# Kernel tuning notes

Measured on AMD Instinct MI355X. Metric: run time of the kernel, lower is better.

## Reference

```python
import jax, jax.numpy as jnp
import numpy as np

BN_EPS = 1e-5
ITER_N = 5

def _bn(x, gamma, beta, mean, var, axis):
    shape = [1] * x.ndim
    shape[axis] = -1
    r = lambda v: v.reshape(shape)
    return (x - r(mean)) * (r(gamma) / jnp.sqrt(r(var) + BN_EPS)) + r(beta)

def _covpool(x):
    # x: (B, d, M); MPNCOV CovpoolLayer: y = x @ I_hat @ x^T, I_hat = (1/M)I - (1/M^2)11^T
    M = x.shape[-1]
    I_hat = (-1.0 / (M * M)) * jnp.ones((M, M), x.dtype) + (1.0 / M) * jnp.eye(M, dtype=x.dtype)
    return jnp.einsum('bdm,mn,ben->bde', x, I_hat, x)

def _sqrtm_ns(A, iterN=ITER_N):
    # MPNCOV SqrtmLayer: trace-normalized Newton-Schulz iteration
    d = A.shape[-1]
    I3 = 3.0 * jnp.eye(d, dtype=A.dtype)
    normA = jnp.trace(A, axis1=1, axis2=2) / 3.0          # (B,)
    A_n = A / normA[:, None, None]
    ZY = 0.5 * (I3 - A_n)
    Y = A_n @ ZY
    Z = ZY
    for _ in range(iterN - 2):
        ZY = 0.5 * (I3 - Z @ Y)
        Y = Y @ ZY
        Z = ZY @ Z
    YZY = 0.5 * (Y @ (I3 - Z @ Y))
    return YZY * jnp.sqrt(normA)[:, None, None]

def setup_inputs() -> dict:
    key = jax.random.key(0)
    ks = jax.random.split(key, 12)
    B, C, H, W = 64, 1024, 16, 16
    D, R = 128, H * W  # att_dim, sp_reso
    return {
        'x': jax.random.normal(ks[0], (B, C, H, W), jnp.float32),
        'w_dr': jax.random.normal(ks[1], (D, C), jnp.float32) * 0.02,
        'b_dr': jax.random.normal(ks[2], (D,), jnp.float32) * 0.02,
        'bn1_gamma': jnp.ones((D,), jnp.float32),
        'bn1_beta': jnp.zeros((D,), jnp.float32),
        'bn1_mean': jax.random.normal(ks[3], (D,), jnp.float32) * 0.1,
        'bn1_var': jax.random.uniform(ks[4], (D,), jnp.float32, 0.5, 1.5),
        'bn2_gamma': jnp.ones((R,), jnp.float32),
        'bn2_beta': jnp.zeros((R,), jnp.float32),
        'bn2_mean': jax.random.normal(ks[5], (R,), jnp.float32) * 0.1,
        'bn2_var': jax.random.uniform(ks[6], (R,), jnp.float32, 0.5, 1.5),
        'rc_w': jax.random.normal(ks[7], (R,), jnp.float32) * 0.1 + 1.0,
        'rc_b': jax.random.normal(ks[8], (R,), jnp.float32) * 0.02,
        'fc_w': jax.random.normal(ks[9], (R, R * R), jnp.float32) * 0.004,
        'fc_b': jax.random.normal(ks[10], (R,), jnp.float32) * 0.02,
    }

def reference(x, w_dr, b_dr, bn1_gamma, bn1_beta, bn1_mean, bn1_var,
              bn2_gamma, bn2_beta, bn2_mean, bn2_var, rc_w, rc_b, fc_w, fc_b):
    B, C, H, W = x.shape
    # 1x1 dimension-reduction conv + BN + ReLU
    y = jnp.einsum('bchw,dc->bdhw', x, w_dr) + b_dr[None, :, None, None]
    y = jax.nn.relu(_bn(y, bn1_gamma, bn1_beta, bn1_mean, bn1_var, axis=1))
    # (B, D, HW) -> (B, HW, D): HW spatial positions as 'channels', D as samples
    y = y.reshape(B, -1, H * W).transpose(0, 2, 1)
    cov = _covpool(y)                  # (B, HW, HW)
    s = _sqrtm_ns(cov, ITER_N)         # (B, HW, HW)
    # row BN over first HW axis (channels of the (B, HW, HW, 1) view)
    s = _bn(s, bn2_gamma, bn2_beta, bn2_mean, bn2_var, axis=1)
    # grouped (depthwise) 1x1 row conv: per-row scale + bias
    s = s * rc_w[None, :, None] + rc_b[None, :, None]
    att = jax.nn.sigmoid(s.reshape(B, -1) @ fc_w.T + fc_b)   # (B, HW)
    att = att.reshape(B, 1, H, W)
    return x * att
```

## Files before the change

### kernel.cpp

```cpp
#include <hip/hip_runtime.h>

typedef unsigned short u16;
typedef unsigned int   u32;
typedef __attribute__((ext_vector_type(8))) short bf8;
typedef __attribute__((ext_vector_type(4))) float f4;
typedef __attribute__((ext_vector_type(16))) float f16f;

#define MFMA(a,b,c)   __builtin_amdgcn_mfma_f32_16x16x32_bf16(a,b,c,0,0,0)
#define MFMA32(a,b,c) __builtin_amdgcn_mfma_f32_32x32x16_bf16(a,b,c,0,0,0)

__device__ __forceinline__ u16 f2bf(float f){
  u32 u = __float_as_uint(f);
  u += 0x7fffu + ((u >> 16) & 1u);
  return (u16)(u >> 16);
}
__device__ __forceinline__ float bf2f(u16 h){ return __uint_as_float(((u32)h) << 16); }
__device__ __forceinline__ u32 pk2(float a, float b){ return (u32)f2bf(a) | ((u32)f2bf(b) << 16); }

__device__ __forceinline__ bf8 ldsFrag(const char* m, int row0, int k0, int pitch){
  int l = threadIdx.x & 63;
  int r = row0 + (l & 15);
  int kb = ((k0 + ((l >> 4) << 3)) << 1) ^ ((r & 7) << 4);
  return *(const bf8*)(m + r * pitch + kb);
}
__device__ __forceinline__ void ldsPut(char* m, int row, int col, int pitch, u16 v){
  int kb = (col << 1) ^ ((row & 7) << 4);
  *(u16*)(m + row * pitch + kb) = v;
}

__device__ __forceinline__ bf8 fragNS(const char* m, int r0, int ks, int l){
  int r = r0 + (l & 31);
  int kb = ((ks << 5) + ((l >> 5) << 4)) ^ ((r & 15) << 4);
  return *(const bf8*)(m + r * 256 + kb);
}
__device__ __forceinline__ bf8 fragWT(const char* m, int r0, int ks, int l){
  int r = r0 + (l & 31);
  int kb = ((ks << 5) + ((l >> 5) << 4)) ^ ((r & 15) << 4);
  return *(const bf8*)(m + r * 512 + kb);
}
__device__ __forceinline__ char* nsAddr(char* m, int row, int col4){
  return m + row * 256 + ((col4 << 1) ^ ((row & 15) << 4));
}

__device__ __forceinline__ void mmPass(const char* A, const char* B, f16f (&acc)[2][2],
                                       int R0, int C0, int l){
  #pragma unroll
  for (int ks = 0; ks < 8; ++ks){
    bf8 a0 = fragNS(A, R0,      ks, l);
    bf8 a1 = fragNS(A, R0 + 32, ks, l);
    bf8 b0 = fragNS(B, C0,      ks, l);
    bf8 b1 = fragNS(B, C0 + 32, ks, l);
    acc[0][0] = MFMA32(a0, b0, acc[0][0]); acc[0][1] = MFMA32(a0, b1, acc[0][1]);
    acc[1][0] = MFMA32(a1, b0, acc[1][0]); acc[1][1] = MFMA32(a1, b1, acc[1][1]);
  }
}

__device__ __forceinline__ void writeTile(char* D, const f16f (&acc)[2][2], int R0, int C0, int l,
                                          float scale, float dval, const uint2* adv){
  #pragma unroll
  for (int ri = 0; ri < 2; ++ri)
  #pragma unroll
  for (int ci = 0; ci < 2; ++ci)
  #pragma unroll
  for (int g = 0; g < 4; ++g){
    int srow = C0 + ci * 32 + (l & 31);
    int scol = R0 + ri * 32 + g * 8 + ((l >> 5) << 2);
    float v[4];
    #pragma unroll
    for (int q = 0; q < 4; ++q){
      float x = scale * acc[ri][ci][g * 4 + q];
      x += ((scol + q) == srow) ? dval : 0.f;
      v[q] = x;
    }
    if (adv){
      uint2 ad = adv[(ri * 2 + ci) * 4 + g];
      v[0] += 1.5f * bf2f((u16)ad.x);
      v[1] += 1.5f * bf2f((u16)(ad.x >> 16));
      v[2] += 1.5f * bf2f((u16)ad.y);
      v[3] += 1.5f * bf2f((u16)(ad.y >> 16));
    }
    *(uint2*)nsAddr(D, srow, scol) = make_uint2(pk2(v[0], v[1]), pk2(v[2], v[3]));
  }
}

__global__ __launch_bounds__(256) void k_prep(const float* __restrict__ wdr,
                                              float* __restrict__ logits,
                                              u16* __restrict__ prep){
  int i = blockIdx.x * 256 + threadIdx.x;
  if (i < 16384) logits[i] = 0.f;
  #pragma unroll
  for (int j = 0; j < 2; ++j){
    int e = i + j * 65536;
    int chunk = e >> 13, rem = e & 8191, d = rem >> 6, cb2 = rem & 63;
    int c = ((cb2 * 2) ^ ((d & 7) << 4)) >> 1;
    prep[e] = f2bf(wdr[d * 1024 + chunk * 64 + c]);
  }
}

__global__ __launch_bounds__(512) void k_conv(
    const u16* __restrict__ wprep, const float* __restrict__ x, const float* __restrict__ bdr,
    const float* __restrict__ g1, const float* __restrict__ be1,
    const float* __restrict__ m1, const float* __restrict__ v1,
    u16* __restrict__ Wg, u16* __restrict__ WTg){
  __shared__ union {
    struct { u16 A[2][8192]; u16 Bt[2][2048]; } s;
    struct { float y[128 * 33]; float musum[512]; float mu[32]; } e;
  } sm;
  int t = threadIdx.x;
  int b = blockIdx.x >> 3, hw0 = (blockIdx.x & 7) * 32;
  const float* xb = x + (size_t)b * 262144 + hw0;

  int w = t >> 6, l = t & 63;
  int d0 = (w >> 1) * 32, hh = (w & 1) * 16;
  int lc = l & 15, lr = (l >> 4) * 4;

  const f4 fz = {0.f, 0.f, 0.f, 0.f};
  f4 acc[2]; acc[0] = fz; acc[1] = fz;

  int cp = t >> 5, hwl = t & 31;

  uint4 ar0, ar1;
  float br0, br1, br2, br3;
  { const uint4* s4 = (const uint4*)wprep;
    ar0 = s4[t]; ar1 = s4[t + 512];
    br0 = xb[(size_t)(2 * cp)      * 256 + hwl];
    br1 = xb[(size_t)(2 * cp + 1)  * 256 + hwl];
    br2 = xb[(size_t)(2 * cp + 32) * 256 + hwl];
    br3 = xb[(size_t)(2 * cp + 33) * 256 + hwl];
  }

  for (int k = 0; k < 16; ++k){
    int cur = k & 1;
    *(uint4*)(sm.s.A[cur] + t * 8)        = ar0;
    *(uint4*)(sm.s.A[cur] + 4096 + t * 8) = ar1;
    { int b0 = (4 * cp) ^ ((hwl & 7) << 4);
      int b1 = (4 * cp + 64) ^ ((hwl & 7) << 4);
      *(u32*)((char*)sm.s.Bt[cur] + hwl * 128 + b0) = pk2(br0, br1);
      *(u32*)((char*)sm.s.Bt[cur] + hwl * 128 + b1) = pk2(br2, br3);
    }
    __syncthreads();
    if (k < 15){
      const uint4* s4 = (const uint4*)(wprep + (k + 1) * 8192);
      ar0 = s4[t]; ar1 = s4[t + 512];
      int c0 = (k + 1) * 64;
      br0 = xb[(size_t)(c0 + 2 * cp)      * 256 + hwl];
      br1 = xb[(size_t)(c0 + 2 * cp + 1)  * 256 + hwl];
      br2 = xb[(size_t)(c0 + 2 * cp + 32) * 256 + hwl];
      br3 = xb[(size_t)(c0 + 2 * cp + 33) * 256 + hwl];
    }
    #pragma unroll
    for (int ks = 0; ks < 2; ++ks){
      int k0 = ks * 32;
      bf8 a0 = ldsFrag((const char*)sm.s.A[cur], d0,      k0, 128);
      bf8 a1 = ldsFrag((const char*)sm.s.A[cur], d0 + 16, k0, 128);
      bf8 b0 = ldsFrag((const char*)sm.s.Bt[cur], hh, k0, 128);
      acc[0] = MFMA(a0, b0, acc[0]);
      acc[1] = MFMA(a1, b0, acc[1]);
    }
    __syncthreads();
  }

  #pragma unroll
  for (int i = 0; i < 2; ++i)
    #pragma unroll
    for (int r = 0; r < 4; ++r){
      int d = d0 + i * 16 + lr + r;
      float s1 = g1[d] * rsqrtf(v1[d] + 1e-5f);
      float t1 = (bdr[d] - m1[d]) * s1 + be1[d];
      int hwp = hh + lc;
      sm.e.y[d * 33 + hwp] = fmaxf(acc[i][r] * s1 + t1, 0.f);
    }
  __syncthreads();
  {
    int part = t >> 5, col = t & 31;
    float s = 0.f;
    #pragma unroll
    for (int i2 = 0; i2 < 8; ++i2) s += sm.e.y[(part * 8 + i2) * 33 + col];
    sm.e.musum[part * 32 + col] = s;
  }
  __syncthreads();
  if (t < 32){
    float m = 0.f;
    #pragma unroll
    for (int p = 0; p < 16; ++p) m += sm.e.musum[p * 32 + t];
    sm.e.mu[t] = m * (1.0f / 128.0f);
  }
  __syncthreads();
  const float ISM = 0.08838834764831845f;
  {
    int hwp = t >> 4, dc = (t & 15) * 8;
    float muv = sm.e.mu[hwp];
    u32 q[4];
    #pragma unroll
    for (int jj = 0; jj < 4; ++jj){
      float a = (sm.e.y[(dc + 2 * jj)     * 33 + hwp] - muv) * ISM;
      float c = (sm.e.y[(dc + 2 * jj + 1) * 33 + hwp] - muv) * ISM;
      q[jj] = pk2(a, c);
    }
    *(uint4*)(Wg + ((size_t)(b * 256 + hw0 + hwp) * 128 + dc)) = make_uint4(q[0], q[1], q[2], q[3]);
  }
  {
    int d = t >> 2, hc = (t & 3) * 8;
    u32 q[4];
    #pragma unroll
    for (int jj = 0; jj < 4; ++jj){
      int h0 = hc + 2 * jj, h1 = hc + 2 * jj + 1;
      float a = (sm.e.y[d * 33 + h0] - sm.e.mu[h0]) * ISM;
      float c = (sm.e.y[d * 33 + h1] - sm.e.mu[h1]) * ISM;
      q[jj] = pk2(a, c);
    }
    *(uint4*)(WTg + ((size_t)(b * 128 + d) * 256 + hw0 + hc)) = make_uint4(q[0], q[1], q[2], q[3]);
  }
}

extern __shared__ char smns[];
__global__ __launch_bounds__(512, 2) void k_ns(const u16* __restrict__ WT,
                                               u16* __restrict__ yf, float* __restrict__ normAg){
  int b = blockIdx.x, t = threadIdx.x;
  char* Yb = smns;
  char* Zb = smns + 32768;
  char* T1 = smns + 65536;
  char* T2 = smns + 98304;
  char* T3 = smns + 131072;
  char* WTl = smns + 65536;
  char* G   = T3;
  float* trp = (float*)smns;

  int w = t >> 6, l = t & 63;
  int wq = w & 3;
  int R0 = (wq >> 1) * 64, C0 = (wq & 1) * 64;

  { const u16* src = WT + (size_t)b * 32768;
    int row = t >> 2, q = t & 3;
    #pragma unroll
    for (int j = 0; j < 8; ++j) {
      int c16 = q + j * 4;
      bf8 v = *(const bf8*)(src + row * 256 + c16 * 8);
      int ph = c16 ^ (row & 15);
      *(bf8*)(WTl + row * 512 + ph * 16) = v;
    }
  }
  if (t == 0) *trp = 0.f;
  __syncthreads();

  int R0g = (w & 3) * 32, C0g = (w >> 2) * 64;
  const f16f fz16 = {};
  f16f gac[2]; gac[0] = fz16; gac[1] = fz16;
  #pragma unroll
  for (int ks = 0; ks < 16; ++ks){
    bf8 a  = fragWT(WTl, R0g,      ks, l);
    bf8 b0 = fragWT(WTl, C0g,      ks, l);
    bf8 b1 = fragWT(WTl, C0g + 32, ks, l);
    gac[0] = MFMA32(a, b0, gac[0]);
    gac[1] = MFMA32(a, b1, gac[1]);
  }
  float tp = 0.f;
  #pragma unroll
  for (int ci = 0; ci < 2; ++ci)
    #pragma unroll
    for (int e = 0; e < 16; ++e){
      int row = R0g + (e & 3) + 8 * (e >> 2) + ((l >> 5) << 2);
      int col = C0g + ci * 32 + (l & 31);
      if (row == col) tp += gac[ci][e];
    }
  #pragma unroll
  for (int off = 32; off > 0; off >>= 1) tp += __shfl_down(tp, off);
  if (l == 0) atomicAdd(trp, tp);
  __syncthreads();

  float normA = fmaxf(*trp / 3.0f, 1e-12f);
  if (t == 0) normAg[b] = normA;
  float inv = 1.0f / normA;
  #pragma unroll
  for (int ci = 0; ci < 2; ++ci)
    #pragma unroll
    for (int g = 0; g < 4; ++g){
      int srow = C0g + ci * 32 + (l & 31);
      int scol = R0g + g * 8 + ((l >> 5) << 2);
      float v0 = gac[ci][g * 4 + 0] * inv, v1 = gac[ci][g * 4 + 1] * inv;
      float v2 = gac[ci][g * 4 + 2] * inv, v3 = gac[ci][g * 4 + 3] * inv;
      *(uint2*)nsAddr(G, srow, scol) = make_uint2(pk2(v0, v1), pk2(v2, v3));
    }
  __syncthreads();

  bf8 gA[8], gB[8];
  #pragma unroll
  for (int ks = 0; ks < 8; ++ks){
    gA[ks] = fragNS(G, C0,      ks, l);
    gB[ks] = fragNS(G, C0 + 32, ks, l);
  }
  { int row = t >> 2, q4 = t & 3;
    #pragma unroll
    for (int j = 0; j < 4; ++j){
      int c16 = q4 * 4 + j;
      int ph = c16 ^ (row & 15);
      bf8 gg = *(const bf8*)(G + row * 256 + ph * 16);
      bf8 yv, zv;
      #pragma unroll
      for (int e = 0; e < 8; ++e){
        int col = c16 * 8 + e;
        float y = -0.5f * bf2f((u16)gg[e]) + ((col == row) ? 1.5f : 0.f);
        yv[e] = (short)f2bf(y);
        zv[e] = (col == row) ? (short)f2bf(-0.5f) : (short)0;
      }
      *(bf8*)(Yb + row * 256 + ph * 16) = yv;
      *(bf8*)(Zb + row * 256 + ph * 16) = zv;
    }
  }
  __syncthreads();

  float z0 = 1.5f;
  for (int it = 0; it < 4; ++it){
    {
      f16f acc[2][2]; acc[0][0] = fz16; acc[0][1] = fz16; acc[1][0] = fz16; acc[1][1] = fz16;
      const char* As = (w < 4) ? Zb : Yb;
      #pragma unroll
      for (int ks = 0; ks < 8; ++ks){
        bf8 a0 = fragNS(As, R0,      ks, l);
        bf8 a1 = fragNS(As, R0 + 32, ks, l);
        acc[0][0] = MFMA32(a0, gA[ks], acc[0][0]); acc[0][1] = MFMA32(a0, gB[ks], acc[0][1]);
        acc[1][0] = MFMA32(a1, gA[ks], acc[1][0]); acc[1][1] = MFMA32(a1, gB[ks], acc[1][1]);
      }
      writeTile((w < 4) ? T1 : T3, acc, R0, C0, l, 1.0f, (w < 4) ? z0 : 0.f, nullptr);
    }
    __syncthreads();

    uint2 adv[16];
    {
      const char* addsrc = (w < 4) ? Zb : Yb;
      #pragma unroll
      for (int ri = 0; ri < 2; ++ri)
      #pragma unroll
      for (int ci = 0; ci < 2; ++ci)
      #pragma unroll
      for (int g = 0; g < 4; ++g){
        int srow = C0 + ci * 32 + (l & 31);
        int scol = R0 + ri * 32 + g * 8 + ((l >> 5) << 2);
        adv[(ri * 2 + ci) * 4 + g] = *(const uint2*)nsAddr((char*)addsrc, srow, scol);
      }
      if (w < 4){
        f16f acc[2][2]; acc[0][0] = fz16; acc[0][1] = fz16; acc[1][0] = fz16; acc[1][1] = fz16;
        mmPass(T1, Yb, acc, R0, C0, l);
        writeTile(T2, acc, R0, C0, l, -0.5f, 0.f, nullptr);
      }
    }
    __syncthreads();

    if ((w >= 4) || (it < 3)){
      f16f acc[2][2]; acc[0][0] = fz16; acc[0][1] = fz16; acc[1][0] = fz16; acc[1][1] = fz16;
      const char* A3 = (w < 4) ? T2 : T3;
      const char* B3 = (w < 4) ? T1 : T2;
      mmPass(A3, B3, acc, R0, C0, l);
      writeTile((w < 4) ? Zb : Yb, acc, R0, C0, l, 1.0f, 0.f, adv);
    }
    __syncthreads();
    z0 *= 1.5f;
  }

  { int row = t >> 2, q = t & 3;
    u16* dst = yf + (size_t)b * 16384 + row * 128;
    #pragma unroll
    for (int j = 0; j < 4; ++j) {
      int c16 = q * 4 + j;
      int ph = c16 ^ (row & 15);
      *(bf8*)(dst + c16 * 8) = *(const bf8*)(Yb + row * 256 + ph * 16);
    }
  }
}

extern __shared__ char smex[];
__global__ __launch_bounds__(512) void k_expand(
    const u16* __restrict__ Wg, const u16* __restrict__ yf, const float* __restrict__ normAg,
    const float* __restrict__ g2, const float* __restrict__ be2, const float* __restrict__ m2,
    const float* __restrict__ v2, const float* __restrict__ rcw, const float* __restrict__ rcb,
    u16* __restrict__ sp){
  int blk = blockIdx.x, b = blk >> 2, iband = blk & 3;
  char* Bm = smex;
  char* Yl = smex + 65536;
  char* El = smex + 98304;
  int t = threadIdx.x;
  { const u16* src = Wg + (size_t)b * 32768;
    int row = t >> 1, q = t & 1;
    #pragma unroll
    for (int j = 0; j < 8; ++j) {
      int c16 = q + j * 2;
      bf8 v = *(const bf8*)(src + row * 128 + c16 * 8);
      int ph = c16 ^ (row & 7);
      *(bf8*)(Bm + row * 256 + ph * 16) = v;
    } }
  { const u16* src = yf + (size_t)b * 16384;
    int row = t >> 2, q = t & 3;
    #pragma unroll
    for (int j = 0; j < 4; ++j) {
      int c16 = q + j * 4;
      bf8 v = *(const bf8*)(src + row * 128 + c16 * 8);
      int ph = c16 ^ (row & 7);
      *(bf8*)(Yl + row * 256 + ph * 16) = v;
    } }
  __syncthreads();
  int w = t >> 6, l = t & 63, lc = l & 15, lr = (l >> 4) * 4;
  const f4 fz = {0.f, 0.f, 0.f, 0.f};
  { int r0 = (w >> 2) * 32, c0 = (w & 3) * 32;
    f4 acc[2][2];
    acc[0][0] = fz; acc[0][1] = fz; acc[1][0] = fz; acc[1][1] = fz;
    #pragma unroll
    for (int kk = 0; kk < 4; ++kk) {
      int k0 = kk * 32;
      bf8 a0 = ldsFrag(Bm, iband * 64 + r0,      k0, 256);
      bf8 a1 = ldsFrag(Bm, iband * 64 + r0 + 16, k0, 256);
      bf8 b0 = ldsFrag(Yl, c0,      k0, 256);
      bf8 b1 = ldsFrag(Yl, c0 + 16, k0, 256);
      acc[0][0] = MFMA(a0, b0, acc[0][0]); acc[0][1] = MFMA(a0, b1, acc[0][1]);
      acc[1][0] = MFMA(a1, b0, acc[1][0]); acc[1][1] = MFMA(a1, b1, acc[1][1]);
    }
    #pragma unroll
    for (int i = 0; i < 2; ++i)
      #pragma unroll
      for (int j = 0; j < 2; ++j)
        #pragma unroll
        for (int r = 0; r < 4; ++r)
          ldsPut(El, r0 + i * 16 + lr + r, c0 + j * 16 + lc, 256, f2bf(acc[i][j][r]));
  }
  __syncthreads();
  { float invs = rsqrtf(normAg[b]);
    int r0 = (w >> 2) * 32, c0 = (w & 3) * 64;
    f4 acc[2][4];
    #pragma unroll
    for (int i = 0; i < 2; ++i)
      #pragma unroll
      for (int j = 0; j < 4; ++j) acc[i][j] = fz;
    #pragma unroll
    for (int kk = 0; kk < 4; ++kk) {
      int k0 = kk * 32;
      bf8 a0 = ldsFrag(El, r0,      k0, 256);
      bf8 a1 = ldsFrag(El, r0 + 16, k0, 256);
      bf8 b0 = ldsFrag(Bm, c0,      k0, 256);
      bf8 b1 = ldsFrag(Bm, c0 + 16, k0, 256);
      bf8 b2 = ldsFrag(Bm, c0 + 32, k0, 256);
      bf8 b3 = ldsFrag(Bm, c0 + 48, k0, 256);
      acc[0][0] = MFMA(a0, b0, acc[0][0]); acc[0][1] = MFMA(a0, b1, acc[0][1]);
      acc[0][2] = MFMA(a0, b2, acc[0][2]); acc[0][3] = MFMA(a0, b3, acc[0][3]);
      acc[1][0] = MFMA(a1, b0, acc[1][0]); acc[1][1] = MFMA(a1, b1, acc[1][1]);
      acc[1][2] = MFMA(a1, b2, acc[1][2]); acc[1][3] = MFMA(a1, b3, acc[1][3]);
    }
    #pragma unroll
    for (int i = 0; i < 2; ++i)
      #pragma unroll
      for (int r = 0; r < 4; ++r) {
        int il = r0 + i * 16 + lr + r;
        int ig = iband * 64 + il;
        float bs = g2[ig] * rsqrtf(v2[ig] + 1e-5f);
        float al = bs * rcw[ig];
        float be = (be2[ig] - m2[ig] * bs) * rcw[ig] + rcb[ig];
        #pragma unroll
        for (int j = 0; j < 4; ++j) {
          int jg = c0 + j * 16 + lc;
          sp[(size_t)b * 65536 + ig * 256 + jg] = f2bf(acc[i][j][r] * invs * al + be);
        }
      }
  }
}

extern __shared__ char smfc[];
__global__ __launch_bounds__(512) void k_fc(const u16* __restrict__ sp,
                                            const float* __restrict__ fcw,
                                            float* __restrict__ logits){
  int kc = blockIdx.x >> 1, rh = blockIdx.x & 1;
  int k0 = kc * 256, rbase = rh * 128;
  char* Al = smfc;
  char* Bl = smfc + 32768;
  int t = threadIdx.x;
  { int row = t >> 3, q = t & 7;
    #pragma unroll
    for (int j = 0; j < 4; ++j) {
      int c16 = q + j * 8;
      bf8 v = *(const bf8*)(sp + (size_t)row * 65536 + k0 + c16 * 8);
      int ph = c16 ^ (row & 7);
      *(bf8*)(Al + row * 512 + ph * 16) = v;
    } }
  { int lane16 = t & 15;
    #pragma unroll
    for (int pass = 0; pass < 4; ++pass) {
      int row = (t >> 4) + pass * 32;
      #pragma unroll
      for (int j = 0; j < 4; ++j) {
        int k = lane16 * 4 + j * 64;
        float4 v = *(const float4*)(fcw + (size_t)(rbase + row) * 65536 + k0 + k);
        int off = (k * 2) ^ ((row & 7) << 4);
        *(u32*)(Bl + row * 512 + off)     = pk2(v.x, v.y);
        *(u32*)(Bl + row * 512 + off + 4) = pk2(v.z, v.w);
      }
    } }
  __syncthreads();
  int w = t >> 6, l = t & 63, lc = l & 15, lr = (l >> 4) * 4;
  int r0 = (w >> 2) * 32, c0 = (w & 3) * 32;
  const f4 fz = {0.f, 0.f, 0.f, 0.f};
  f4 acc[2][2];
  acc[0][0] = fz; acc[0][1] = fz; acc[1][0] = fz; acc[1][1] = fz;
  #pragma unroll
  for (int kk = 0; kk < 8; ++kk) {
    int ks = kk * 32;
    bf8 a0 = ldsFrag(Al, r0,      ks, 512);
    bf8 a1 = ldsFrag(Al, r0 + 16, ks, 512);
    bf8 b0 = ldsFrag(Bl, c0,      ks, 512);
    bf8 b1 = ldsFrag(Bl, c0 + 16, ks, 512);
    acc[0][0] = MFMA(a0, b0, acc[0][0]); acc[0][1] = MFMA(a0, b1, acc[0][1]);
    acc[1][0] = MFMA(a1, b0, acc[1][0]); acc[1][1] = MFMA(a1, b1, acc[1][1]);
  }
  #pragma unroll
  for (int i = 0; i < 2; ++i)
    #pragma unroll
    for (int j = 0; j < 2; ++j)
      #pragma unroll
      for (int r = 0; r < 4; ++r) {
        int row = r0 + i * 16 + lr + r;
        int col = rbase + c0 + j * 16 + lc;
        atomicAdd(logits + row * 256 + col, acc[i][j][r]);
      }
}

__global__ __launch_bounds__(256) void k_mul(const float* __restrict__ x,
                                             const float* __restrict__ logits,
                                             const float* __restrict__ fcb,
                                             float* __restrict__ out, int n4){
  int i = blockIdx.x * 256 + threadIdx.x;
  int str = gridDim.x * 256;
  for (; i < n4; i += str) {
    int e = i << 2;
    int b = e >> 18;
    int hw = e & 255;
    float4 xv = ((const float4*)x)[i];
    float4 lg = *(const float4*)(logits + (b << 8) + hw);
    float4 fb = *(const float4*)(fcb + hw);
    float4 o;
    o.x = xv.x / (1.f + expf(-(lg.x + fb.x)));
    o.y = xv.y / (1.f + expf(-(lg.y + fb.y)));
    o.z = xv.z / (1.f + expf(-(lg.z + fb.z)));
    o.w = xv.w / (1.f + expf(-(lg.w + fb.w)));
    ((float4*)out)[i] = o;
  }
}

extern "C" void kernel_launch(void* const* d_in, const int* in_sizes, int n_in,
                              void* d_out, int out_size, void* d_ws, size_t ws_size,
                              hipStream_t stream){
  const float* x   = (const float*)d_in[0];
  const float* wdr = (const float*)d_in[1];
  const float* bdr = (const float*)d_in[2];
  const float* g1  = (const float*)d_in[3];
  const float* be1 = (const float*)d_in[4];
  const float* m1  = (const float*)d_in[5];
  const float* v1  = (const float*)d_in[6];
  const float* g2  = (const float*)d_in[7];
  const float* be2 = (const float*)d_in[8];
  const float* m2  = (const float*)d_in[9];
  const float* v2  = (const float*)d_in[10];
  const float* rcw = (const float*)d_in[11];
  const float* rcb = (const float*)d_in[12];
  const float* fcw = (const float*)d_in[13];
  const float* fcb = (const float*)d_in[14];
  float* out = (float*)d_out;
  char* ws = (char*)d_ws;
  u16*   Wg  = (u16*)(ws);
  u16*   WTg = (u16*)(ws + (4u  << 20));
  u16*   yfg = (u16*)(ws + (8u  << 20));
  float* nAg = (float*)(ws + (10u << 20));
  u16*   wpr = (u16*)(ws + (10u << 20) + 4096);
  u16*   spg = (u16*)(ws + (11u << 20));
  float* lgt = (float*)(ws + (20u << 20));

  hipFuncSetAttribute((const void*)k_ns,     hipFuncAttributeMaxDynamicSharedMemorySize, 163840);
  hipFuncSetAttribute((const void*)k_expand, hipFuncAttributeMaxDynamicSharedMemorySize, 114688);
  hipFuncSetAttribute((const void*)k_fc,     hipFuncAttributeMaxDynamicSharedMemorySize, 98304);

  k_prep  <<<256,  256, 0,      stream>>>(wdr, lgt, wpr);
  k_conv  <<<512,  512, 0,      stream>>>(wpr, x, bdr, g1, be1, m1, v1, Wg, WTg);
  k_ns    <<<64,   512, 163840, stream>>>(WTg, yfg, nAg);
  k_expand<<<256,  512, 114688, stream>>>(Wg, yfg, nAg, g2, be2, m2, v2, rcw, rcb, spg);
  k_fc    <<<512,  512, 98304,  stream>>>(spg, fcw, lgt);
  k_mul   <<<2048, 256, 0,      stream>>>(x, lgt, fcb, out, 4194304);
}
```

Before: 115.7 us.

## Stream weight tiles into LDS with direct global-to-LDS loads and manual waitcnt

Replaces the register-staged copy of the weight tile with global_load_lds (direct global-to-LDS) loads issued two stages ahead, and manually controls vmcnt waits and barriers with sched_barrier fences. The loop is fully unrolled so each iteration can use a fixed wait count. The aim is to cut VGPR staging and LDS store instructions and to overlap the weight fetch with MFMA work in the dimension-reduction GEMM stage. In exchange, correctness now depends on hand-counted outstanding loads and barrier placement, and the double-buffer reuse is fragile if the load ordering differs from what the wait counts assume.

```diff
diff --git a/kernel.cpp b/kernel.cpp
--- a/kernel.cpp
+++ b/kernel.cpp
@@ -16,6 +16,11 @@
 }
 __device__ __forceinline__ float bf2f(u16 h){ return __uint_as_float(((u32)h) << 16); }
 __device__ __forceinline__ u32 pk2(float a, float b){ return (u32)f2bf(a) | ((u32)f2bf(b) << 16); }
+
+__device__ __forceinline__ void glds16(const u16* g, u16* l){
+  __builtin_amdgcn_global_load_lds((const __attribute__((address_space(1))) u32*)g,
+                                   (__attribute__((address_space(3))) u32*)l, 16, 0, 0);
+}
 
 __device__ __forceinline__ bf8 ldsFrag(const char* m, int row0, int k0, int pitch){
   int l = threadIdx.x & 63;
@@ -118,47 +123,59 @@
   f4 acc[2]; acc[0] = fz; acc[1] = fz;
 
   int cp = t >> 5, hwl = t & 31;
-
-  uint4 ar0, ar1;
-  float br0, br1, br2, br3;
-  { const uint4* s4 = (const uint4*)wprep;
-    ar0 = s4[t]; ar1 = s4[t + 512];
-    br0 = xb[(size_t)(2 * cp)      * 256 + hwl];
-    br1 = xb[(size_t)(2 * cp + 1)  * 256 + hwl];
-    br2 = xb[(size_t)(2 * cp + 32) * 256 + hwl];
-    br3 = xb[(size_t)(2 * cp + 33) * 256 + hwl];
-  }
-
+  int bo0 = (4 * cp) ^ ((hwl & 7) << 4);
+  int bo1 = (4 * cp + 64) ^ ((hwl & 7) << 4);
+
+  glds16(wprep + t * 8,        sm.s.A[0] + t * 8);
+  glds16(wprep + 4096 + t * 8, sm.s.A[0] + 4096 + t * 8);
+  glds16(wprep + 8192 + t * 8,        sm.s.A[1] + t * 8);
+  glds16(wprep + 8192 + 4096 + t * 8, sm.s.A[1] + 4096 + t * 8);
+  float br0 = xb[(size_t)(2 * cp)      * 256 + hwl];
+  float br1 = xb[(size_t)(2 * cp + 1)  * 256 + hwl];
+  float br2 = xb[(size_t)(2 * cp + 32) * 256 + hwl];
+  float br3 = xb[(size_t)(2 * cp + 33) * 256 + hwl];
+
+  #pragma unroll
   for (int k = 0; k < 16; ++k){
-    int cur = k & 1;
-    *(uint4*)(sm.s.A[cur] + t * 8)        = ar0;
-    *(uint4*)(sm.s.A[cur] + 4096 + t * 8) = ar1;
-    { int b0 = (4 * cp) ^ ((hwl & 7) << 4);
-      int b1 = (4 * cp + 64) ^ ((hwl & 7) << 4);
-      *(u32*)((char*)sm.s.Bt[cur] + hwl * 128 + b0) = pk2(br0, br1);
-      *(u32*)((char*)sm.s.Bt[cur] + hwl * 128 + b1) = pk2(br2, br3);
-    }
-    __syncthreads();
+    if (k >= 1 && k < 15){
+      const u16* src = wprep + (k + 1) * 8192;
+      glds16(src + t * 8,        sm.s.A[(k + 1) & 1] + t * 8);
+      glds16(src + 4096 + t * 8, sm.s.A[(k + 1) & 1] + 4096 + t * 8);
+    }
+    float nb0 = 0.f, nb1 = 0.f, nb2 = 0.f, nb3 = 0.f;
     if (k < 15){
-      const uint4* s4 = (const uint4*)(wprep + (k + 1) * 8192);
-      ar0 = s4[t]; ar1 = s4[t + 512];
       int c0 = (k + 1) * 64;
-      br0 = xb[(size_t)(c0 + 2 * cp)      * 256 + hwl];
-      br1 = xb[(size_t)(c0 + 2 * cp + 1)  * 256 + hwl];
-      br2 = xb[(size_t)(c0 + 2 * cp + 32) * 256 + hwl];
-      br3 = xb[(size_t)(c0 + 2 * cp + 33) * 256 + hwl];
-    }
+      nb0 = xb[(size_t)(c0 + 2 * cp)      * 256 + hwl];
+      nb1 = xb[(size_t)(c0 + 2 * cp + 1)  * 256 + hwl];
+      nb2 = xb[(size_t)(c0 + 2 * cp + 32) * 256 + hwl];
+      nb3 = xb[(size_t)(c0 + 2 * cp + 33) * 256 + hwl];
+    }
+    __builtin_amdgcn_sched_barrier(0);
+    if (k == 0)       asm volatile("s_waitcnt vmcnt(4)" ::: "memory");
+    else if (k == 15) asm volatile("s_waitcnt vmcnt(0)" ::: "memory");
+    else              asm volatile("s_waitcnt vmcnt(6)" ::: "memory");
+    __builtin_amdgcn_sched_barrier(0);
+    *(u32*)((char*)sm.s.Bt[k & 1] + hwl * 128 + bo0) = pk2(br0, br1);
+    *(u32*)((char*)sm.s.Bt[k & 1] + hwl * 128 + bo1) = pk2(br2, br3);
+    asm volatile("s_waitcnt lgkmcnt(0)" ::: "memory");
+    __builtin_amdgcn_sched_barrier(0);
+    __builtin_amdgcn_s_barrier();
+    __builtin_amdgcn_sched_barrier(0);
     #pragma unroll
     for (int ks = 0; ks < 2; ++ks){
       int k0 = ks * 32;
-      bf8 a0 = ldsFrag((const char*)sm.s.A[cur], d0,      k0, 128);
-      bf8 a1 = ldsFrag((const char*)sm.s.A[cur], d0 + 16, k0, 128);
-      bf8 b0 = ldsFrag((const char*)sm.s.Bt[cur], hh, k0, 128);
+      bf8 a0 = ldsFrag((const char*)sm.s.A[k & 1], d0,      k0, 128);
+      bf8 a1 = ldsFrag((const char*)sm.s.A[k & 1], d0 + 16, k0, 128);
+      bf8 b0 = ldsFrag((const char*)sm.s.Bt[k & 1], hh, k0, 128);
       acc[0] = MFMA(a0, b0, acc[0]);
       acc[1] = MFMA(a1, b0, acc[1]);
     }
-    __syncthreads();
-  }
+    __builtin_amdgcn_sched_barrier(0);
+    __builtin_amdgcn_s_barrier();
+    __builtin_amdgcn_sched_barrier(0);
+    br0 = nb0; br1 = nb1; br2 = nb2; br3 = nb3;
+  }
+  __syncthreads();
 
   #pragma unroll
   for (int i = 0; i < 2; ++i)
```

Measured after the change: 113.7 us. About the same (-1.7%).
